# Kernel tuning notes

Measured on AMD Instinct MI355X. Metric: run time of the kernel, lower is better.

The kernel has to match this reference:

```python
import jax, jax.numpy as jnp
import numpy as np

E = 1024        # embed_dim
NH = 16         # num_heads
HD = E // NH    # head_dim = 64
MLP = 4096
HID = int(2 * MLP / 3)  # 2730, TransNeXt ConvGLU hidden
NT = 1          # no_rope task tokens (skip rotary / skip dwconv)
B, S = 8, 1025
GRID = 32       # sqrt(S - NT)
EPS = 1e-6
SCALE = HD ** -0.5


def rmsnorm(x, g):
    return x * jax.lax.rsqrt(jnp.mean(x * x, axis=-1, keepdims=True) + EPS) * g


def apply_rope(t):
    # t: [B, NH, s, HD] -- rotate-half RoPE over image-token positions
    s = t.shape[2]
    pos = jnp.arange(s, dtype=jnp.float32)
    inv_freq = 1.0 / (10000.0 ** (jnp.arange(0, HD, 2, dtype=jnp.float32) / HD))
    freqs = pos[:, None] * inv_freq[None, :]          # [s, HD/2]
    cos = jnp.concatenate([jnp.cos(freqs)] * 2, -1)   # [s, HD]
    sin = jnp.concatenate([jnp.sin(freqs)] * 2, -1)
    t1, t2 = jnp.split(t, 2, axis=-1)
    rot = jnp.concatenate([-t2, t1], axis=-1)
    return t * cos + rot * sin


def rope_skip_task(t):
    # first NT tokens are task tokens -> identity; rest get rotary with positions 0..
    return jnp.concatenate([t[:, :, :NT], apply_rope(t[:, :, NT:])], axis=2)


def setup_inputs() -> dict:
    key = jax.random.key(0)
    ks = jax.random.split(key, 12)
    init = lambda k, shape, fan: (jax.random.normal(k, shape, jnp.float32) * (fan ** -0.5))
    return {
        "x": jax.random.normal(ks[0], (B, S, E), jnp.float32),
        "g1": jnp.ones((E,), jnp.float32),
        "w_qkv": init(ks[1], (E, 3 * E), E),
        "b_qkv": jnp.zeros((3 * E,), jnp.float32),
        "w_proj": init(ks[2], (E, E), E),
        "b_proj": jnp.zeros((E,), jnp.float32),
        "g2": jnp.ones((E,), jnp.float32),
        "fc1_w": init(ks[3], (E, 2 * HID), E),
        "fc1_b": jnp.zeros((2 * HID,), jnp.float32),
        "dw_w": init(ks[4], (3, 3, 1, HID), 9),  # HWIO depthwise 3x3
        "dw_b": jnp.zeros((HID,), jnp.float32),
        "fc2_w": init(ks[5], (HID, E), HID),
        "fc2_b": jnp.zeros((E,), jnp.float32),
    }


def reference(x, g1, w_qkv, b_qkv, w_proj, b_proj, g2, fc1_w, fc1_b, dw_w, dw_b, fc2_w, fc2_b):
    # ---- attention block ----
    residual = x
    xn = rmsnorm(x, g1)
    qkv = xn @ w_qkv + b_qkv                              # [B,S,3E]
    qkv = qkv.reshape(B, S, 3, NH, HD).transpose(2, 0, 3, 1, 4)
    q, k, v = qkv[0], qkv[1], qkv[2]                      # [B,NH,S,HD]
    q = rope_skip_task(q)
    k = rope_skip_task(k)
    attn = jnp.einsum("bhqd,bhkd->bhqk", q * SCALE, k)    # [B,NH,S,S]
    attn = jax.nn.softmax(attn, axis=-1)
    out = jnp.einsum("bhqk,bhkd->bhqd", attn, v)          # [B,NH,S,HD]
    out = out.transpose(0, 2, 1, 3).reshape(B, S, E)
    out = out @ w_proj + b_proj
    x = residual + out

    # ---- ConvGLU MLP block ----
    residual = x
    xn = rmsnorm(x, g2)
    h = xn @ fc1_w + fc1_b                                # [B,S,2*HID]
    xg, vg = jnp.split(h, 2, axis=-1)
    x_task, x_img = xg[:, :NT], xg[:, NT:]                # dwconv only on image tokens
    img = x_img.reshape(B, GRID, GRID, HID)
    img = jax.lax.conv_general_dilated(
        img, dw_w, window_strides=(1, 1), padding="SAME",
        feature_group_count=HID,
        dimension_numbers=("NHWC", "HWIO", "NHWC")) + dw_b
    x_img = img.reshape(B, GRID * GRID, HID)
    xc = jnp.concatenate([x_task, x_img], axis=1)
    h = jax.nn.gelu(xc, approximate=False) * vg           # GLU gate
    h = h @ fc2_w + fc2_b
    return residual + h
```

## Files before the change

kernel.cpp:

```cpp
#include <hip/hip_runtime.h>
#include <hip/hip_bf16.h>
#include <math.h>

#define E_DIM 1024
#define NHEAD 16
#define HID_DIM 2730
#define KP_FC2 2752
#define HB_LD 5504
#define B_DIM 8
#define S_DIM 1025
#define EPS_V 1e-6f
#define SCALE_V 0.125f
#define MROWS (B_DIM * S_DIM)

typedef __attribute__((ext_vector_type(8))) short short8;
typedef __attribute__((ext_vector_type(4))) float f32x4;
typedef unsigned short us;

__device__ __forceinline__ float b2f(us u) {
    union { unsigned int i; float f; } x; x.i = ((unsigned int)u) << 16; return x.f;
}
__device__ __forceinline__ us f2b(float f) {
    __hip_bfloat16 h = __float2bfloat16(f);
    return *reinterpret_cast<us*>(&h);
}

__device__ __forceinline__ void stage16(const void* g, void* l) {
    __builtin_amdgcn_global_load_lds(
        (const __attribute__((address_space(1))) unsigned int*)g,
        (__attribute__((address_space(3))) unsigned int*)l,
        16, 0, 0);
}

__device__ __forceinline__ int sl(int row, int c8) {
    return (row * 8 + (c8 ^ (row & 7))) * 8;
}

#define MFMA16(a, b, c) __builtin_amdgcn_mfma_f32_16x16x32_bf16(a, b, c, 0, 0, 0)

__global__ __launch_bounds__(256) void rmsnorm_kernel(const float* __restrict__ x,
        const float* __restrict__ g, us* __restrict__ out) {
    int row = blockIdx.x;
    const float4* xr = (const float4*)(x + (size_t)row * E_DIM);
    float4 v = xr[threadIdx.x];
    float ss = v.x*v.x + v.y*v.y + v.z*v.z + v.w*v.w;
    #pragma unroll
    for (int off = 32; off > 0; off >>= 1) ss += __shfl_down(ss, off, 64);
    __shared__ float wsum[4];
    int lane = threadIdx.x & 63, w = threadIdx.x >> 6;
    if (lane == 0) wsum[w] = ss;
    __syncthreads();
    float tot = wsum[0] + wsum[1] + wsum[2] + wsum[3];
    float inv = rsqrtf(tot * (1.0f / E_DIM) + EPS_V);
    float4 gv = ((const float4*)g)[threadIdx.x];
    ushort4 o;
    o.x = f2b(v.x * inv * gv.x); o.y = f2b(v.y * inv * gv.y);
    o.z = f2b(v.z * inv * gv.z); o.w = f2b(v.w * inv * gv.w);
    ((ushort4*)(out + (size_t)row * E_DIM))[threadIdx.x] = o;
}

__global__ __launch_bounds__(256) void convt_kernel(const float* __restrict__ W,
        us* __restrict__ WT, int K, int N, int KPad, int swap_half) {
    __shared__ float T[32][33];
    int n0 = blockIdx.x * 32, k0 = blockIdx.y * 32;
    int c = threadIdx.x & 31, r4 = (threadIdx.x >> 5) << 2;
    #pragma unroll
    for (int i = 0; i < 4; i++) {
        int k = k0 + r4 + i, n = n0 + c;
        int src = n;
        if (swap_half && n < N) src = (n < swap_half) ? n + swap_half : n - swap_half;
        T[c][r4 + i] = (k < K && n < N) ? W[(size_t)k * N + src] : 0.0f;
    }
    __syncthreads();
    #pragma unroll
    for (int i = 0; i < 4; i++) {
        int n = n0 + r4 + i, k = k0 + c;
        if (n < N && k < KPad) WT[(size_t)n * KPad + k] = f2b(T[r4 + i][c]);
    }
}

__global__ __launch_bounds__(256) void bias_perm_kernel(const float* __restrict__ b,
        float* __restrict__ bp) {
    int r = blockIdx.x * 256 + threadIdx.x;
    if (r < 2 * HID_DIM) bp[r] = b[r < HID_DIM ? r + HID_DIM : r - HID_DIM];
}

template<bool BF16OUT>
__global__ __launch_bounds__(512, 2) void gemm256(const us* __restrict__ A, int lda,
        const us* __restrict__ Bt, int ldb, const float* __restrict__ bias,
        const float* __restrict__ Rres, void* __restrict__ Cv,
        int M, int N, int K, int ldc) {
    __shared__ __align__(16) us lds[2][4][8192];
    us* const L = &lds[0][0][0];
    const int tid = threadIdx.x;
    const int lane = tid & 63;
    const int w = tid >> 6;
    const int wm = w >> 2, wn = w & 3;
    const int l15 = lane & 15, quad = lane >> 4;
    const int m0 = blockIdx.y * 256, n0 = blockIdx.x * 256;

    const int r0 = tid >> 3;
    const int c80 = (tid & 7) ^ (r0 & 7);
    const us* const pA = A + (size_t)(m0 + r0) * lda + c80 * 8;
    const us* const pB = Bt + (size_t)(n0 + r0) * ldb + c80 * 8;
    const size_t a64 = (size_t)64 * lda, b64 = (size_t)64 * ldb;
    us* const dst = L + tid * 8;

#define STG_A(b, h, kt) do { \
    const us* s_ = pA + (size_t)(h) * 2 * a64 + (size_t)(kt) * 64; \
    stage16(s_,       dst + ((b) * 4 + (h)) * 8192); \
    stage16(s_ + a64, dst + ((b) * 4 + (h)) * 8192 + 4096); \
} while (0)
#define STG_B(b, h, kt) do { \
    const us* s_ = pB + (size_t)(h) * 2 * b64 + (size_t)(kt) * 64; \
    stage16(s_,       dst + ((b) * 4 + 2 + (h)) * 8192); \
    stage16(s_ + b64, dst + ((b) * 4 + 2 + (h)) * 8192 + 4096); \
} while (0)

    f32x4 acc[8][4];
    #pragma unroll
    for (int m = 0; m < 8; m++)
        #pragma unroll
        for (int n = 0; n < 4; n++) acc[m][n] = (f32x4){0.f, 0.f, 0.f, 0.f};

    const int nk = K >> 6;

    STG_A(0, 0, 0); STG_A(0, 1, 0);
    STG_B(0, 0, 0); STG_B(0, 1, 0);
    STG_B(1, 0, 1); STG_B(1, 1, 1);
    asm volatile("s_waitcnt vmcnt(4)" ::: "memory");
    __builtin_amdgcn_s_barrier();

    const int brow = (wn & 1) * 64;
    for (int t = 0; t < nk; t++) {
        const int c = t & 1, cn = c ^ 1;
        const us* aB = L + (c * 4 + wm) * 8192;
        const us* bB = L + (c * 4 + 2 + (wn >> 1)) * 8192;
        short8 bf[4][2];
        #pragma unroll
        for (int n = 0; n < 4; n++) {
            bf[n][0] = *(const short8*)(bB + sl(brow + n * 16 + l15, quad));
            bf[n][1] = *(const short8*)(bB + sl(brow + n * 16 + l15, 4 + quad));
        }
        #pragma unroll
        for (int p = 0; p < 4; p++) {
            const int mp = 2 * p;
            short8 a00 = *(const short8*)(aB + sl(mp * 16 + l15, quad));
            short8 a01 = *(const short8*)(aB + sl(mp * 16 + l15, 4 + quad));
            short8 a10 = *(const short8*)(aB + sl(mp * 16 + 16 + l15, quad));
            short8 a11 = *(const short8*)(aB + sl(mp * 16 + 16 + l15, 4 + quad));
            if (p == 0) {
                if (t + 1 < nk) { STG_A(cn, 0, t + 1); STG_A(cn, 1, t + 1); }
            } else if (p == 1) {
                if (t + 2 < nk) STG_B(c, 0, t + 2);
            } else if (p == 2) {
                if (t + 2 < nk) STG_B(c, 1, t + 2);
            }
            __builtin_amdgcn_s_barrier();
            __builtin_amdgcn_s_setprio(1);
            #pragma unroll
            for (int n = 0; n < 4; n++) {
                acc[mp][n]     = MFMA16(a00, bf[n][0], acc[mp][n]);
                acc[mp][n]     = MFMA16(a01, bf[n][1], acc[mp][n]);
                acc[mp + 1][n] = MFMA16(a10, bf[n][0], acc[mp + 1][n]);
                acc[mp + 1][n] = MFMA16(a11, bf[n][1], acc[mp + 1][n]);
            }
            __builtin_amdgcn_s_setprio(0);
            if (p == 3) {
                if (t + 2 >= nk) { asm volatile("s_waitcnt vmcnt(0)" ::: "memory"); }
                else             { asm volatile("s_waitcnt vmcnt(4)" ::: "memory"); }
            }
            __builtin_amdgcn_s_barrier();
        }
    }

    #pragma unroll
    for (int m = 0; m < 8; m++) {
        int gm0 = m0 + wm * 128 + m * 16 + quad * 4;
        #pragma unroll
        for (int n = 0; n < 4; n++) {
            int gn = n0 + wn * 64 + n * 16 + l15;
            if (gn >= N) continue;
            float bs = bias[gn];
            #pragma unroll
            for (int r = 0; r < 4; r++) {
                int gm = gm0 + r;
                if (gm >= M) continue;
                float v = acc[m][n][r] + bs;
                if (BF16OUT) {
                    ((us*)Cv)[(size_t)gm * ldc + gn] = f2b(v);
                } else {
                    ((float*)Cv)[(size_t)gm * ldc + gn] = v + Rres[(size_t)gm * ldc + gn];
                }
            }
        }
    }
#undef STG_A
#undef STG_B
}

__global__ __launch_bounds__(256) void rope_kernel(us* __restrict__ qkv) {
    int idx = blockIdx.x * 256 + threadIdx.x;
    int i = idx & 31;
    int h = (idx >> 5) & (NHEAD - 1);
    int rc = idx >> 9;
    int s = rc % S_DIM;
    us* q = qkv + (size_t)rc * 3072 + h * 64;
    us* k = q + 1024;
    if (s == 0) {
        q[i] = f2b(b2f(q[i]) * SCALE_V);
        q[i + 32] = f2b(b2f(q[i + 32]) * SCALE_V);
        return;
    }
    float pos = (float)(s - 1);
    float invf = expf((float)i * (-9.210340371976184f / 32.0f));
    float f = pos * invf;
    float c = cosf(f), sn = sinf(f);
    float q1 = b2f(q[i]), q2 = b2f(q[i + 32]);
    q[i]      = f2b((q1 * c - q2 * sn) * SCALE_V);
    q[i + 32] = f2b((q2 * c + q1 * sn) * SCALE_V);
    float k1 = b2f(k[i]), k2 = b2f(k[i + 32]);
    k[i]      = f2b(k1 * c - k2 * sn);
    k[i + 32] = f2b(k2 * c + k1 * sn);
}

__global__ __launch_bounds__(256) void vtrans_kernel(const us* __restrict__ qkv,
        us* __restrict__ Vt) {
    __shared__ us T[64][65];
    int st = blockIdx.x, h = blockIdx.y, bc = blockIdx.z;
    int tid = threadIdx.x;
    int r = tid & 63, cb = (tid >> 6) * 16;
    const us* src = qkv + (size_t)(bc * S_DIM + st * 64 + r) * 3072 + 2048 + h * 64 + cb;
    #pragma unroll
    for (int i = 0; i < 4; i++) {
        ushort4 v = *(const ushort4*)(src + i * 4);
        T[cb + i*4 + 0][r] = v.x; T[cb + i*4 + 1][r] = v.y;
        T[cb + i*4 + 2][r] = v.z; T[cb + i*4 + 3][r] = v.w;
    }
    __syncthreads();
    int d = tid >> 2, sc = (tid & 3) * 16;
    us* dstp = Vt + ((size_t)((bc * 16 + h) * 64 + d)) * 1088 + st * 64 + sc;
    #pragma unroll
    for (int g = 0; g < 4; g++) {
        ushort4 o;
        int i0 = sc + g * 4;
        o.x = (st*64 + i0 + 0 < S_DIM) ? T[d][i0 + 0] : 0;
        o.y = (st*64 + i0 + 1 < S_DIM) ? T[d][i0 + 1] : 0;
        o.z = (st*64 + i0 + 2 < S_DIM) ? T[d][i0 + 2] : 0;
        o.w = (st*64 + i0 + 3 < S_DIM) ? T[d][i0 + 3] : 0;
        *(ushort4*)(dstp + g * 4) = o;
    }
}

__global__ __launch_bounds__(256) void attn_kernel(const us* __restrict__ qkv,
        const us* __restrict__ Vt, us* __restrict__ attnb) {
    __shared__ __align__(16) us Qs[4096];
    __shared__ __align__(16) us Ks[4096];
    __shared__ __align__(16) us Vts[4096];
    __shared__ __align__(16) us Ps[4096];
    int qt = blockIdx.x, h = blockIdx.y, bc = blockIdx.z;
    int tid = threadIdx.x;
    int lane = tid & 63, w = tid >> 6;
    int l15 = lane & 15, quad = lane >> 4;

    const us* qg = qkv + (size_t)(bc * S_DIM + qt * 64) * 3072 + h * 64;
    #pragma unroll
    for (int i = 0; i < 2; i++) {
        int slot = i * 256 + tid;
        int row = slot >> 3, c8 = (slot & 7) ^ (row & 7);
        stage16(qg + (size_t)row * 3072 + c8 * 8, Qs + slot * 8);
    }
    const us* kg = qkv + (size_t)(bc * S_DIM) * 3072 + 1024 + h * 64;
    const us* vgp = Vt + (size_t)((bc * 16 + h) * 64) * 1088;

    f32x4 acc_o[4];
    float mr[4], lr[4];
    #pragma unroll
    for (int r = 0; r < 4; r++) { mr[r] = -1e30f; lr[r] = 0.f; }
    #pragma unroll
    for (int j = 0; j < 4; j++) acc_o[j] = (f32x4){0.f, 0.f, 0.f, 0.f};

    for (int kt = 0; kt < 17; kt++) {
        __syncthreads();
        #pragma unroll
        for (int i = 0; i < 2; i++) {
            int slot = i * 256 + tid;
            int row = slot >> 3, c8 = (slot & 7) ^ (row & 7);
            stage16(kg + (size_t)(kt * 64 + row) * 3072 + c8 * 8, Ks + slot * 8);
            stage16(vgp + (size_t)row * 1088 + kt * 64 + c8 * 8, Vts + slot * 8);
        }
        __syncthreads();

        f32x4 accS[4];
        #pragma unroll
        for (int j = 0; j < 4; j++) accS[j] = (f32x4){0.f, 0.f, 0.f, 0.f};
        short8 qa0 = *(const short8*)(Qs + sl(16 * w + l15, quad));
        short8 qa1 = *(const short8*)(Qs + sl(16 * w + l15, 4 + quad));
        #pragma unroll
        for (int j = 0; j < 4; j++) {
            short8 kb0 = *(const short8*)(Ks + sl(16 * j + l15, quad));
            short8 kb1 = *(const short8*)(Ks + sl(16 * j + l15, 4 + quad));
            accS[j] = __builtin_amdgcn_mfma_f32_16x16x32_bf16(qa0, kb0, accS[j], 0, 0, 0);
            accS[j] = __builtin_amdgcn_mfma_f32_16x16x32_bf16(qa1, kb1, accS[j], 0, 0, 0);
        }
        float pr[4][4];
        #pragma unroll
        for (int j = 0; j < 4; j++) {
            if (kt * 64 + 16 * j + l15 >= S_DIM) {
                #pragma unroll
                for (int r = 0; r < 4; r++) accS[j][r] = -1e30f;
            }
        }
        #pragma unroll
        for (int r = 0; r < 4; r++) {
            float tm = fmaxf(fmaxf(accS[0][r], accS[1][r]), fmaxf(accS[2][r], accS[3][r]));
            #pragma unroll
            for (int off = 1; off < 16; off <<= 1)
                tm = fmaxf(tm, __shfl_xor(tm, off, 64));
            float mnew = fmaxf(mr[r], tm);
            float al = __expf(mr[r] - mnew);
            mr[r] = mnew;
            float rs = 0.f;
            #pragma unroll
            for (int j = 0; j < 4; j++) {
                float p = __expf(accS[j][r] - mnew);
                pr[j][r] = p;
                rs += p;
            }
            #pragma unroll
            for (int off = 1; off < 16; off <<= 1)
                rs += __shfl_xor(rs, off, 64);
            lr[r] = lr[r] * al + rs;
            #pragma unroll
            for (int j = 0; j < 4; j++) acc_o[j][r] *= al;
        }
        #pragma unroll
        for (int j = 0; j < 4; j++) {
            #pragma unroll
            for (int r = 0; r < 4; r++) {
                int prow = quad * 4 + r;
                int idx = sl(16 * w + prow, 2 * j + (l15 >> 3)) + (l15 & 7);
                Ps[idx] = f2b(pr[j][r]);
            }
        }
        short8 pa0 = *(const short8*)(Ps + sl(16 * w + l15, quad));
        short8 pa1 = *(const short8*)(Ps + sl(16 * w + l15, 4 + quad));
        #pragma unroll
        for (int j = 0; j < 4; j++) {
            short8 vb0 = *(const short8*)(Vts + sl(16 * j + l15, quad));
            short8 vb1 = *(const short8*)(Vts + sl(16 * j + l15, 4 + quad));
            acc_o[j] = __builtin_amdgcn_mfma_f32_16x16x32_bf16(pa0, vb0, acc_o[j], 0, 0, 0);
            acc_o[j] = __builtin_amdgcn_mfma_f32_16x16x32_bf16(pa1, vb1, acc_o[j], 0, 0, 0);
        }
    }
    #pragma unroll
    for (int r = 0; r < 4; r++) {
        int s = qt * 64 + 16 * w + quad * 4 + r;
        if (s >= S_DIM) continue;
        float invl = 1.0f / lr[r];
        #pragma unroll
        for (int j = 0; j < 4; j++)
            attnb[(size_t)(bc * S_DIM + s) * E_DIM + h * 64 + 16 * j + l15] =
                f2b(acc_o[j][r] * invl);
    }
}

__global__ __launch_bounds__(256) void conv_gelu_kernel(us* __restrict__ hb,
        const float* __restrict__ dw_w, const float* __restrict__ dw_b) {
    int p = blockIdx.x % S_DIM;
    size_t row = blockIdx.x;
    size_t brow = row - p;
    for (int c = threadIdx.x; c < HID_DIM; c += 256) {
        float val;
        if (p == 0) {
            val = b2f(hb[row * HB_LD + HID_DIM + c]);
        } else {
            int pp = p - 1;
            int gy = pp >> 5, gx = pp & 31;
            float a = dw_b[c];
            #pragma unroll
            for (int dy = 0; dy < 3; dy++) {
                int ny = gy + dy - 1;
                if (ny < 0 || ny >= 32) continue;
                #pragma unroll
                for (int dx = 0; dx < 3; dx++) {
                    int nx = gx + dx - 1;
                    if (nx < 0 || nx >= 32) continue;
                    a = fmaf(b2f(hb[(brow + 1 + ny * 32 + nx) * HB_LD + HID_DIM + c]),
                             dw_w[(dy * 3 + dx) * HID_DIM + c], a);
                }
            }
            val = a;
        }
        float ge = 0.5f * val * (1.0f + erff(val * 0.70710678118654752f));
        hb[row * HB_LD + c] = f2b(ge * b2f(hb[row * HB_LD + c]));
    }
}

static size_t ws_need(int cb) {
    size_t R = (size_t)cb * 1025, Rp = ((R + 127) / 128) * 128;
    size_t end1 = Rp*1024*2 + Rp*3072*2 + (size_t)cb*16*64*1088*2
                + 8320ull*1024*2 + 3072ull*1024*2 + 1024ull*1024*2;
    size_t end2 = Rp*1024*2 + Rp*HB_LD*2 + 5504ull*1024*2 + 1024ull*KP_FC2*2 + 5460*4;
    return end1 > end2 ? end1 : end2;
}

extern "C" void kernel_launch(void* const* d_in, const int* in_sizes, int n_in,
                              void* d_out, int out_size, void* d_ws, size_t ws_size,
                              hipStream_t stream) {
    const float* x      = (const float*)d_in[0];
    const float* g1     = (const float*)d_in[1];
    const float* w_qkv  = (const float*)d_in[2];
    const float* b_qkv  = (const float*)d_in[3];
    const float* w_proj = (const float*)d_in[4];
    const float* b_proj = (const float*)d_in[5];
    const float* g2     = (const float*)d_in[6];
    const float* fc1_w  = (const float*)d_in[7];
    const float* fc1_b  = (const float*)d_in[8];
    const float* dw_w   = (const float*)d_in[9];
    const float* dw_b   = (const float*)d_in[10];
    const float* fc2_w  = (const float*)d_in[11];
    const float* fc2_b  = (const float*)d_in[12];
    float* out = (float*)d_out;
    char* base = (char*)d_ws;

    int CB = 2;
    if (ws_size >= ws_need(8)) CB = 8;
    else if (ws_size >= ws_need(4)) CB = 4;
    int NC = B_DIM / CB;
    size_t R = (size_t)CB * 1025, Rp = ((R + 127) / 128) * 128;
    int gy256 = (int)((R + 255) / 256);

    us* xn    = (us*)base;
    size_t o  = Rp * 1024 * 2;
    us* qkv   = (us*)(base + o);
    us* hbuf  = (us*)(base + o);
    size_t o2 = o + Rp * 3072 * 2;
    us* Vt    = (us*)(base + o2);
    size_t o3 = o2 + (size_t)CB * 16 * 64 * 1088 * 2;
    us* attnb = (us*)(base + o3);
    size_t o4 = o3 + 8320ull * 1024 * 2;
    us* qkvT  = (us*)(base + o4);
    size_t o5 = o4 + 3072ull * 1024 * 2;
    us* projT = (us*)(base + o5);
    size_t p2 = o + Rp * HB_LD * 2;
    us* fc1T  = (us*)(base + p2);
    size_t p3 = p2 + 5504ull * 1024 * 2;
    us* fc2T  = (us*)(base + p3);
    float* fc1bp = (float*)(base + p3 + 1024ull * KP_FC2 * 2);

    convt_kernel<<<dim3(96, 32), 256, 0, stream>>>(w_qkv, qkvT, 1024, 3072, 1024, 0);
    convt_kernel<<<dim3(32, 32), 256, 0, stream>>>(w_proj, projT, 1024, 1024, 1024, 0);
    for (int c = 0; c < NC; c++) {
        size_t roff = (size_t)c * R;
        rmsnorm_kernel<<<(int)R, 256, 0, stream>>>(x + roff * E_DIM, g1, xn);
        gemm256<true><<<dim3(12, gy256), 512, 0, stream>>>(xn, 1024, qkvT, 1024,
                b_qkv, nullptr, qkv, (int)R, 3072, 1024, 3072);
        rope_kernel<<<(int)(2 * R), 256, 0, stream>>>(qkv);
        vtrans_kernel<<<dim3(17, 16, CB), 256, 0, stream>>>(qkv, Vt);
        attn_kernel<<<dim3(17, 16, CB), 256, 0, stream>>>(qkv, Vt, attnb + roff * E_DIM);
    }
    gemm256<false><<<dim3(4, (MROWS + 255) / 256), 512, 0, stream>>>(attnb, 1024,
            projT, 1024, b_proj, x, out, MROWS, 1024, 1024, 1024);

    convt_kernel<<<dim3(171, 32), 256, 0, stream>>>(fc1_w, fc1T, 1024, 5460, 1024, HID_DIM);
    convt_kernel<<<dim3(32, 86), 256, 0, stream>>>(fc2_w, fc2T, HID_DIM, 1024, KP_FC2, 0);
    bias_perm_kernel<<<22, 256, 0, stream>>>(fc1_b, fc1bp);
    for (int c = 0; c < NC; c++) {
        size_t roff = (size_t)c * R;
        float* outc = out + roff * E_DIM;
        rmsnorm_kernel<<<(int)R, 256, 0, stream>>>(outc, g2, xn);
        gemm256<true><<<dim3(22, gy256), 512, 0, stream>>>(xn, 1024, fc1T, 1024,
                fc1bp, nullptr, hbuf, (int)R, 5460, 1024, HB_LD);
        conv_gelu_kernel<<<(int)R, 256, 0, stream>>>(hbuf, dw_w, dw_b);
        gemm256<false><<<dim3(4, gy256), 512, 0, stream>>>(hbuf, HB_LD, fc2T, KP_FC2,
                fc2_b, outc, outc, (int)R, 1024, KP_FC2, 1024);
    }
}
```

Measured before the change: 876.7 us.

## Double-buffer K/V tiles in attention, keep Q in registers, lazy softmax rescale

```diff
diff --git a/kernel.cpp b/kernel.cpp
--- a/kernel.cpp
+++ b/kernel.cpp
@@ -254,25 +254,25 @@
 
 __global__ __launch_bounds__(256) void attn_kernel(const us* __restrict__ qkv,
         const us* __restrict__ Vt, us* __restrict__ attnb) {
-    __shared__ __align__(16) us Qs[4096];
-    __shared__ __align__(16) us Ks[4096];
-    __shared__ __align__(16) us Vts[4096];
+    __shared__ __align__(16) us Kb[2][4096];
+    __shared__ __align__(16) us Vb[2][4096];
     __shared__ __align__(16) us Ps[4096];
     int qt = blockIdx.x, h = blockIdx.y, bc = blockIdx.z;
     int tid = threadIdx.x;
     int lane = tid & 63, w = tid >> 6;
     int l15 = lane & 15, quad = lane >> 4;
 
-    const us* qg = qkv + (size_t)(bc * S_DIM + qt * 64) * 3072 + h * 64;
-    #pragma unroll
-    for (int i = 0; i < 2; i++) {
-        int slot = i * 256 + tid;
-        int row = slot >> 3, c8 = (slot & 7) ^ (row & 7);
-        stage16(qg + (size_t)row * 3072 + c8 * 8, Qs + slot * 8);
-    }
+    const us* qrow = qkv + (size_t)(bc * S_DIM + qt * 64 + 16 * w + l15) * 3072 + h * 64;
+    short8 qa0 = *(const short8*)(qrow + quad * 8);
+    short8 qa1 = *(const short8*)(qrow + 32 + quad * 8);
+
     const us* kg = qkv + (size_t)(bc * S_DIM) * 3072 + 1024 + h * 64;
     const us* vgp = Vt + (size_t)((bc * 16 + h) * 64) * 1088;
 
+    int s0 = tid, s1 = 256 + tid;
+    int row0 = s0 >> 3, c8_0 = (s0 & 7) ^ (row0 & 7);
+    int row1 = s1 >> 3, c8_1 = (s1 & 7) ^ (row1 & 7);
+
     f32x4 acc_o[4];
     float mr[4], lr[4];
     #pragma unroll
@@ -280,30 +280,34 @@
     #pragma unroll
     for (int j = 0; j < 4; j++) acc_o[j] = (f32x4){0.f, 0.f, 0.f, 0.f};
 
+    stage16(kg + (size_t)row0 * 3072 + c8_0 * 8, Kb[0] + s0 * 8);
+    stage16(vgp + (size_t)row0 * 1088 + c8_0 * 8, Vb[0] + s0 * 8);
+    stage16(kg + (size_t)row1 * 3072 + c8_1 * 8, Kb[0] + (s1 & 255) * 8 + 2048 * 8 * 0 + 256 * 8);
+    stage16(vgp + (size_t)row1 * 1088 + c8_1 * 8, Vb[0] + s1 * 8);
+    __syncthreads();
+
     for (int kt = 0; kt < 17; kt++) {
-        __syncthreads();
-        #pragma unroll
-        for (int i = 0; i < 2; i++) {
-            int slot = i * 256 + tid;
-            int row = slot >> 3, c8 = (slot & 7) ^ (row & 7);
-            stage16(kg + (size_t)(kt * 64 + row) * 3072 + c8 * 8, Ks + slot * 8);
-            stage16(vgp + (size_t)row * 1088 + kt * 64 + c8 * 8, Vts + slot * 8);
-        }
-        __syncthreads();
+        int cur = kt & 1, nxt = cur ^ 1;
+        if (kt + 1 < 17) {
+            stage16(kg + (size_t)((kt + 1) * 64 + row0) * 3072 + c8_0 * 8, Kb[nxt] + s0 * 8);
+            stage16(vgp + (size_t)row0 * 1088 + (kt + 1) * 64 + c8_0 * 8, Vb[nxt] + s0 * 8);
+            stage16(kg + (size_t)((kt + 1) * 64 + row1) * 3072 + c8_1 * 8, Kb[nxt] + s1 * 8);
+            stage16(vgp + (size_t)row1 * 1088 + (kt + 1) * 64 + c8_1 * 8, Vb[nxt] + s1 * 8);
+        }
 
         f32x4 accS[4];
         #pragma unroll
         for (int j = 0; j < 4; j++) accS[j] = (f32x4){0.f, 0.f, 0.f, 0.f};
-        short8 qa0 = *(const short8*)(Qs + sl(16 * w + l15, quad));
-        short8 qa1 = *(const short8*)(Qs + sl(16 * w + l15, 4 + quad));
+        __builtin_amdgcn_s_setprio(1);
         #pragma unroll
         for (int j = 0; j < 4; j++) {
-            short8 kb0 = *(const short8*)(Ks + sl(16 * j + l15, quad));
-            short8 kb1 = *(const short8*)(Ks + sl(16 * j + l15, 4 + quad));
-            accS[j] = __builtin_amdgcn_mfma_f32_16x16x32_bf16(qa0, kb0, accS[j], 0, 0, 0);
-            accS[j] = __builtin_amdgcn_mfma_f32_16x16x32_bf16(qa1, kb1, accS[j], 0, 0, 0);
-        }
-        float pr[4][4];
+            short8 kb0 = *(const short8*)(Kb[cur] + sl(16 * j + l15, quad));
+            short8 kb1 = *(const short8*)(Kb[cur] + sl(16 * j + l15, 4 + quad));
+            accS[j] = MFMA16(qa0, kb0, accS[j]);
+            accS[j] = MFMA16(qa1, kb1, accS[j]);
+        }
+        __builtin_amdgcn_s_setprio(0);
+
         #pragma unroll
         for (int j = 0; j < 4; j++) {
             if (kt * 64 + 16 * j + l15 >= S_DIM) {
@@ -311,28 +315,40 @@
                 for (int r = 0; r < 4; r++) accS[j][r] = -1e30f;
             }
         }
+
+        float tm[4];
         #pragma unroll
         for (int r = 0; r < 4; r++) {
-            float tm = fmaxf(fmaxf(accS[0][r], accS[1][r]), fmaxf(accS[2][r], accS[3][r]));
+            float t = fmaxf(fmaxf(accS[0][r], accS[1][r]), fmaxf(accS[2][r], accS[3][r]));
             #pragma unroll
             for (int off = 1; off < 16; off <<= 1)
-                tm = fmaxf(tm, __shfl_xor(tm, off, 64));
-            float mnew = fmaxf(mr[r], tm);
-            float al = __expf(mr[r] - mnew);
-            mr[r] = mnew;
+                t = fmaxf(t, __shfl_xor(t, off, 64));
+            tm[r] = t;
+        }
+        int need = (tm[0] > mr[0] + 8.f) || (tm[1] > mr[1] + 8.f) ||
+                   (tm[2] > mr[2] + 8.f) || (tm[3] > mr[3] + 8.f);
+        if (__any(need)) {
+            #pragma unroll
+            for (int r = 0; r < 4; r++) {
+                float mnew = fmaxf(mr[r], tm[r]);
+                float al = __expf(mr[r] - mnew);
+                mr[r] = mnew;
+                lr[r] *= al;
+                #pragma unroll
+                for (int j = 0; j < 4; j++) acc_o[j][r] *= al;
+            }
+        }
+        float pr[4][4];
+        #pragma unroll
+        for (int r = 0; r < 4; r++) {
             float rs = 0.f;
             #pragma unroll
             for (int j = 0; j < 4; j++) {
-                float p = __expf(accS[j][r] - mnew);
+                float p = __expf(accS[j][r] - mr[r]);
                 pr[j][r] = p;
                 rs += p;
             }
-            #pragma unroll
-            for (int off = 1; off < 16; off <<= 1)
-                rs += __shfl_xor(rs, off, 64);
-            lr[r] = lr[r] * al + rs;
-            #pragma unroll
-            for (int j = 0; j < 4; j++) acc_o[j][r] *= al;
+            lr[r] += rs;
         }
         #pragma unroll
         for (int j = 0; j < 4; j++) {
@@ -345,13 +361,23 @@
         }
         short8 pa0 = *(const short8*)(Ps + sl(16 * w + l15, quad));
         short8 pa1 = *(const short8*)(Ps + sl(16 * w + l15, 4 + quad));
+        __builtin_amdgcn_s_setprio(1);
         #pragma unroll
         for (int j = 0; j < 4; j++) {
-            short8 vb0 = *(const short8*)(Vts + sl(16 * j + l15, quad));
-            short8 vb1 = *(const short8*)(Vts + sl(16 * j + l15, 4 + quad));
-            acc_o[j] = __builtin_amdgcn_mfma_f32_16x16x32_bf16(pa0, vb0, acc_o[j], 0, 0, 0);
-            acc_o[j] = __builtin_amdgcn_mfma_f32_16x16x32_bf16(pa1, vb1, acc_o[j], 0, 0, 0);
-        }
+            short8 vb0 = *(const short8*)(Vb[cur] + sl(16 * j + l15, quad));
+            short8 vb1 = *(const short8*)(Vb[cur] + sl(16 * j + l15, 4 + quad));
+            acc_o[j] = MFMA16(pa0, vb0, acc_o[j]);
+            acc_o[j] = MFMA16(pa1, vb1, acc_o[j]);
+        }
+        __builtin_amdgcn_s_setprio(0);
+        __syncthreads();
+    }
+
+    #pragma unroll
+    for (int r = 0; r < 4; r++) {
+        #pragma unroll
+        for (int off = 1; off < 16; off <<= 1)
+            lr[r] += __shfl_xor(lr[r], off, 64);
     }
     #pragma unroll
     for (int r = 0; r < 4; r++) {
```

Measured after the change: 841.2 us. 1.04x faster.
